# Kernel optimization log

Hardware: AMD Instinct MI355X
Metric: run time of the kernel (lower is better)

Reference implementation:

```python
import jax, jax.numpy as jnp
import numpy as np

OUTCOMES = [8, 8, 8, 8, 8, 8]           # concept outcome counts (concepts_order)
N_TOTAL = int(np.prod(OUTCOMES))        # 262144 joint states
N_VALID = 8192                          # admissible states
B, D = 4096, 1024


def setup_inputs() -> dict:
    key = jax.random.key(0)
    k1, k2 = jax.random.split(key)
    embeddings = jax.random.normal(k1, (B, D), dtype=jnp.float32)
    W = jax.random.normal(k2, (N_VALID, D), dtype=jnp.float32) * 0.02
    b = jnp.zeros((N_VALID,), dtype=jnp.float32)
    # unique sorted admissible-state indices, like torch.argwhere(mask)
    rng = np.random.default_rng(0)
    valid_states = jnp.asarray(
        np.sort(rng.choice(N_TOTAL, size=N_VALID, replace=False)).astype(np.int32))
    return {"embeddings": embeddings, "W": W, "b": b, "valid_states": valid_states}


def reference(embeddings, W, b, valid_states):
    # softmax over valid states: [B, N_VALID]
    probs = jax.nn.softmax(embeddings @ W.T + b, axis=1)
    probs_t = probs.T  # [N_VALID, B] for leading-axis segment reduction
    marginals = []
    stride = N_TOTAL
    for n_i in OUTCOMES:
        stride //= n_i
        # digit of each valid joint-state index along this concept's axis
        digit = (valid_states // stride) % n_i  # [N_VALID]
        # equivalent to scattering probs into the full joint tensor and
        # summing over all other concept axes, without materializing it
        m = jax.ops.segment_sum(probs_t, digit, num_segments=n_i).T  # [B, n_i]
        marginals.append(m)
    return jnp.stack(marginals)  # [n_concepts, B, 8]
```

## Files before the change

### kernel.cpp

```cpp
#include <hip/hip_runtime.h>
#include <hip/hip_bf16.h>
#include <cstdint>
#include <cstddef>

typedef __bf16 bf16_t;
typedef bf16_t bf16x8 __attribute__((ext_vector_type(8)));
typedef bf16_t bf16x4 __attribute__((ext_vector_type(4)));
typedef float  f32x4  __attribute__((ext_vector_type(4)));
typedef unsigned int u32;

#define BROWS 4096
#define NV    8192
#define KD    1024
#define KSPLIT 16
#define NT    16

#define GLL(gsrc, ldst) \
  __builtin_amdgcn_global_load_lds((const __attribute__((address_space(1))) u32*)(gsrc), \
                                   (__attribute__((address_space(3))) u32*)(ldst), 16, 0, 0)
#define FENCE asm volatile("" ::: "memory")

__global__ void cvt_kernel(const float* __restrict__ src, bf16_t* __restrict__ dst, int n4) {
  int idx = blockIdx.x * blockDim.x + threadIdx.x;
  int stride = gridDim.x * blockDim.x;
  for (int i = idx; i < n4; i += stride) {
    float4 v = ((const float4*)src)[i];
    bf16x4 o;
    o[0] = (bf16_t)v.x; o[1] = (bf16_t)v.y; o[2] = (bf16_t)v.z; o[3] = (bf16_t)v.w;
    ((bf16x4*)dst)[i] = o;
  }
}

__global__ void build_st_kernel(const int* __restrict__ vstate, bf16_t* __restrict__ st) {
  int g = blockIdx.x * blockDim.x + threadIdx.x;
  if (g >= 48 * NV) return;
  int bucket = g >> 13;
  int j = g & (NV - 1);
  int c = bucket >> 3;
  int d = bucket & 7;
  int dig = (vstate[j] >> (15 - 3 * c)) & 7;
  st[g] = (bf16_t)(dig == d ? 1.0f : 0.0f);
}

__global__ __launch_bounds__(512, 2)
void gemm_exp_kernel(const bf16_t* __restrict__ A, const bf16_t* __restrict__ B,
                     const float* __restrict__ bias, bf16_t* __restrict__ expout) {
  __shared__ __align__(16) char lds[2][65536];
  #define AKH0 0
  #define AKH1 16384
  #define BKH0 32768
  #define BKH1 49152

  const int t    = threadIdx.x;
  const int lane = t & 63;
  const int wv   = t >> 6;
  const int wm   = wv >> 2;
  const int wn   = wv & 3;
  const int fr   = lane & 15;
  const int fq   = lane >> 4;

  int bid = blockIdx.x;
  int wg  = (bid & 7) * 64 + (bid >> 3);
  const int mt = wg >> 5;
  const int nt = wg & 31;
  const int row0 = mt * 256;
  const int col0 = nt * 256;

  const int srow = lane >> 2;
  const int skel = ((lane & 3) ^ ((lane >> 3) & 3)) * 8;
  const bf16_t* aptr = A + (size_t)(row0 + wv * 32 + srow) * KD + skel;
  const bf16_t* bptr = B + (size_t)(col0 + wv * 32 + srow) * KD + skel;
  const int dchunk = (wv * 2) * 1024;

  const int xsw = (fr & 6) << 3;
  const int base_a = (((wm * 128 + fr) * 64 + fq * 16) ^ xsw);
  const int base_b = 32768 + (((wn * 64 + fr) * 64 + fq * 16) ^ xsw);

  f32x4 acc[8][4] = {};

  GLL(aptr, &lds[0][AKH0 + dchunk]);
  GLL(aptr + 16 * KD, &lds[0][AKH0 + dchunk + 1024]);
  GLL(bptr, &lds[0][BKH0 + dchunk]);
  GLL(bptr + 16 * KD, &lds[0][BKH0 + dchunk + 1024]);
  GLL(aptr + 32, &lds[0][AKH1 + dchunk]);
  GLL(aptr + 32 + 16 * KD, &lds[0][AKH1 + dchunk + 1024]);
  GLL(bptr + 32, &lds[0][BKH1 + dchunk]);
  GLL(bptr + 32 + 16 * KD, &lds[0][BKH1 + dchunk + 1024]);
  asm volatile("s_waitcnt vmcnt(0)" ::: "memory");
  __builtin_amdgcn_s_barrier();
  FENCE;

  int cur = 0;
  for (int kt = 0; kt < NT; ++kt) {
    const char* bufp = lds[cur];
    char* nbuf = lds[cur ^ 1];
    const bool pf = (kt + 1 < NT);

    bf16x8 a0[8], b0[4], a1[8], b1[4];

#pragma unroll
    for (int n = 0; n < 4; ++n)
      b0[n] = *(const bf16x8*)(bufp + base_b + n * 1024);
#pragma unroll
    for (int m = 0; m < 8; ++m)
      a0[m] = *(const bf16x8*)(bufp + base_a + m * 1024);

    if (pf) {
      const bf16_t* an = aptr + (kt + 1) * 64;
      const bf16_t* bn = bptr + (kt + 1) * 64;
      GLL(an, &nbuf[AKH0 + dchunk]);
      GLL(an + 16 * KD, &nbuf[AKH0 + dchunk + 1024]);
      GLL(bn, &nbuf[BKH0 + dchunk]);
      GLL(bn + 16 * KD, &nbuf[BKH0 + dchunk + 1024]);
      GLL(an + 32, &nbuf[AKH1 + dchunk]);
      GLL(an + 32 + 16 * KD, &nbuf[AKH1 + dchunk + 1024]);
      GLL(bn + 32, &nbuf[BKH1 + dchunk]);
      GLL(bn + 32 + 16 * KD, &nbuf[BKH1 + dchunk + 1024]);
    }

#pragma unroll
    for (int n = 0; n < 4; ++n)
      b1[n] = *(const bf16x8*)(bufp + base_b + 16384 + n * 1024);
#pragma unroll
    for (int m = 0; m < 8; ++m)
      a1[m] = *(const bf16x8*)(bufp + base_a + 16384 + m * 1024);

    __builtin_amdgcn_s_setprio(1);
#pragma unroll
    for (int m = 0; m < 8; ++m)
#pragma unroll
      for (int n = 0; n < 4; ++n)
        acc[m][n] = __builtin_amdgcn_mfma_f32_16x16x32_bf16(a0[m], b0[n], acc[m][n], 0, 0, 0);
#pragma unroll
    for (int m = 0; m < 8; ++m)
#pragma unroll
      for (int n = 0; n < 4; ++n)
        acc[m][n] = __builtin_amdgcn_mfma_f32_16x16x32_bf16(a1[m], b1[n], acc[m][n], 0, 0, 0);
    __builtin_amdgcn_s_setprio(0);

    asm volatile("s_waitcnt vmcnt(0)" ::: "memory");
    __builtin_amdgcn_sched_barrier(0);
    __builtin_amdgcn_s_barrier();
    FENCE;
    cur ^= 1;
  }

#pragma unroll
  for (int n = 0; n < 4; ++n) {
    const int col = col0 + wn * 64 + n * 16 + fr;
    const float bb = bias[col];
#pragma unroll
    for (int m = 0; m < 8; ++m) {
      const int rowb = row0 + wm * 128 + m * 16 + fq * 4;
#pragma unroll
      for (int r = 0; r < 4; ++r) {
        float e = exp2f((acc[m][n][r] + bb) * 1.44269504088896340736f);
        expout[(size_t)(rowb + r) * NV + col] = (bf16_t)e;
      }
    }
  }
}

__global__ __launch_bounds__(256)
void marginal_mfma_kernel(const bf16_t* __restrict__ expbuf, const bf16_t* __restrict__ st,
                          float* __restrict__ part) {
  __shared__ bf16_t sE[128][32];
  __shared__ bf16_t sS[48][32];

  const int t    = threadIdx.x;
  const int lane = t & 63;
  const int wv   = t >> 6;

  const int rt = blockIdx.x >> 4;
  const int ks = blockIdx.x & (KSPLIT - 1);
  const int row0 = rt * 128;
  const int kbase = ks * (NV / KSPLIT);

  const int srow = t >> 2;
  const int skel = (t & 3) * 8;
  const bf16_t* ep0 = expbuf + (size_t)(row0 + srow) * NV + kbase + skel;
  const bf16_t* ep1 = ep0 + (size_t)64 * NV;
  const bf16_t* sp0 = st + (size_t)srow * NV + kbase + skel;
  bf16_t* se0 = &sE[0][0] + (wv * 64) * 8;
  bf16_t* se1 = &sE[0][0] + (256 + wv * 64) * 8;
  bf16_t* ss0 = &sS[0][0] + (wv * 64) * 8;

  const int fr = lane & 15;
  const int fq = lane >> 4;

  f32x4 acc[2][3] = {};

  for (int kk = 0; kk < NV / KSPLIT; kk += 32) {
    GLL(ep0 + kk, se0);
    GLL(ep1 + kk, se1);
    if (wv < 3) GLL(sp0 + kk, ss0);
    __syncthreads();

    bf16x8 af[2], bg[3];
#pragma unroll
    for (int m = 0; m < 2; ++m)
      af[m] = *(const bf16x8*)&sE[wv * 32 + m * 16 + fr][fq * 8];
#pragma unroll
    for (int n = 0; n < 3; ++n)
      bg[n] = *(const bf16x8*)&sS[n * 16 + fr][fq * 8];
#pragma unroll
    for (int m = 0; m < 2; ++m)
#pragma unroll
      for (int n = 0; n < 3; ++n)
        acc[m][n] = __builtin_amdgcn_mfma_f32_16x16x32_bf16(af[m], bg[n], acc[m][n], 0, 0, 0);
    __syncthreads();
  }

  float* pbase = part + (size_t)ks * BROWS * 48;
#pragma unroll
  for (int m = 0; m < 2; ++m) {
    const int rowb = row0 + wv * 32 + m * 16 + fq * 4;
#pragma unroll
    for (int n = 0; n < 3; ++n) {
      const int bucket = n * 16 + fr;
#pragma unroll
      for (int r = 0; r < 4; ++r)
        pbase[(size_t)(rowb + r) * 48 + bucket] = acc[m][n][r];
    }
  }
}

__global__ __launch_bounds__(64)
void reduce_kernel(const float* __restrict__ part, float* __restrict__ out) {
  const int b = blockIdx.x;
  const int t = threadIdx.x;
  __shared__ float fin[48];
  if (t < 48) {
    float s = 0.f;
#pragma unroll
    for (int ks = 0; ks < KSPLIT; ++ks)
      s += part[((size_t)ks * BROWS + b) * 48 + t];
    fin[t] = s;
  }
  __syncthreads();
  if (t < 48) {
    float total = fin[0] + fin[1] + fin[2] + fin[3] + fin[4] + fin[5] + fin[6] + fin[7];
    out[(size_t)(t >> 3) * BROWS * 8 + (size_t)b * 8 + (t & 7)] = fin[t] / total;
  }
}

extern "C" void kernel_launch(void* const* d_in, const int* in_sizes, int n_in,
                              void* d_out, int out_size, void* d_ws, size_t ws_size,
                              hipStream_t stream) {
  const float* E    = (const float*)d_in[0];
  const float* W    = (const float*)d_in[1];
  const float* bias = (const float*)d_in[2];
  const int*   vs   = (const int*)d_in[3];
  float* out = (float*)d_out;

  char* ws = (char*)d_ws;
  size_t off = 0;
  bf16_t* Eb     = (bf16_t*)(ws + off); off += (size_t)BROWS * KD * 2;
  bf16_t* Wb     = (bf16_t*)(ws + off); off += (size_t)NV * KD * 2;
  bf16_t* expbuf = (bf16_t*)(ws + off); off += (size_t)BROWS * NV * 2;
  bf16_t* st     = (bf16_t*)(ws + off); off += (size_t)48 * NV * 2;
  float*  part   = (float*)(ws + off);  off += (size_t)KSPLIT * BROWS * 48 * 4;

  build_st_kernel<<<(48 * NV + 255) / 256, 256, 0, stream>>>(vs, st);
  cvt_kernel<<<2048, 256, 0, stream>>>(E, Eb, BROWS * KD / 4);
  cvt_kernel<<<2048, 256, 0, stream>>>(W, Wb, NV * KD / 4);
  gemm_exp_kernel<<<512, 512, 0, stream>>>(Eb, Wb, bias, expbuf);
  marginal_mfma_kernel<<<32 * KSPLIT, 256, 0, stream>>>(expbuf, st, part);
  reduce_kernel<<<BROWS, 64, 0, stream>>>(part, out);
}
```

Before: 119.6 us.

## Fuse exp and marginal MFMA reduction into GEMM epilogue, drop exp buffer

The GEMM is transposed so each block tiles 256 valid states by 256 batch rows. The epilogue writes exp values into LDS in swizzled form and immediately multiplies them against a swizzled one-hot state-to-bucket matrix with MFMA, producing per-state-tile partial marginals. This removes the 64MB bf16 exp buffer round trip and the separate marginal kernel. In exchange the reduce now sums 32 partials per row instead of 16, and the epilogue adds two LDS passes with barriers.

```diff
diff --git a/kernel.cpp b/kernel.cpp
--- a/kernel.cpp
+++ b/kernel.cpp
@@ -12,8 +12,9 @@
 #define BROWS 4096
 #define NV    8192
 #define KD    1024
-#define KSPLIT 16
 #define NT    16
+#define ST    48
+#define LOG2E 1.44269504088896340736f
 
 #define GLL(gsrc, ldst) \
   __builtin_amdgcn_global_load_lds((const __attribute__((address_space(1))) u32*)(gsrc), \
@@ -31,20 +32,22 @@
   }
 }
 
-__global__ void build_st_kernel(const int* __restrict__ vstate, bf16_t* __restrict__ st) {
+__global__ void build_s2t_kernel(const int* __restrict__ vstate, bf16_t* __restrict__ s2t) {
   int g = blockIdx.x * blockDim.x + threadIdx.x;
-  if (g >= 48 * NV) return;
-  int bucket = g >> 13;
-  int j = g & (NV - 1);
-  int c = bucket >> 3;
-  int d = bucket & 7;
-  int dig = (vstate[j] >> (15 - 3 * c)) & 7;
-  st[g] = (bf16_t)(dig == d ? 1.0f : 0.0f);
+  if (g >= ST * NV) return;
+  int b = g >> 13;
+  int ig = g & (NV - 1);
+  int c = b >> 3;
+  int d = b & 7;
+  int src = ig ^ ((b & 7) << 3);
+  int dig = (vstate[src] >> (15 - 3 * c)) & 7;
+  s2t[g] = (bf16_t)(dig == d ? 1.0f : 0.0f);
 }
 
 __global__ __launch_bounds__(512, 2)
-void gemm_exp_kernel(const bf16_t* __restrict__ A, const bf16_t* __restrict__ B,
-                     const float* __restrict__ bias, bf16_t* __restrict__ expout) {
+void gemm_fused_kernel(const bf16_t* __restrict__ W, const bf16_t* __restrict__ E,
+                       const float* __restrict__ bias, const bf16_t* __restrict__ s2t,
+                       float* __restrict__ part) {
   __shared__ __align__(16) char lds[2][65536];
   #define AKH0 0
   #define AKH1 16384
@@ -61,15 +64,15 @@
 
   int bid = blockIdx.x;
   int wg  = (bid & 7) * 64 + (bid >> 3);
-  const int mt = wg >> 5;
-  const int nt = wg & 31;
-  const int row0 = mt * 256;
-  const int col0 = nt * 256;
+  const int stile = wg >> 4;
+  const int btile = wg & 15;
+  const int st0 = stile * 256;
+  const int bt0 = btile * 256;
 
   const int srow = lane >> 2;
   const int skel = ((lane & 3) ^ ((lane >> 3) & 3)) * 8;
-  const bf16_t* aptr = A + (size_t)(row0 + wv * 32 + srow) * KD + skel;
-  const bf16_t* bptr = B + (size_t)(col0 + wv * 32 + srow) * KD + skel;
+  const bf16_t* aptr = W + (size_t)(st0 + wv * 32 + srow) * KD + skel;
+  const bf16_t* bptr = E + (size_t)(bt0 + wv * 32 + srow) * KD + skel;
   const int dchunk = (wv * 2) * 1024;
 
   const int xsw = (fr & 6) << 3;
@@ -145,83 +148,58 @@
     cur ^= 1;
   }
 
-#pragma unroll
-  for (int n = 0; n < 4; ++n) {
-    const int col = col0 + wn * 64 + n * 16 + fr;
-    const float bb = bias[col];
-#pragma unroll
-    for (int m = 0; m < 8; ++m) {
-      const int rowb = row0 + wm * 128 + m * 16 + fq * 4;
-#pragma unroll
-      for (int r = 0; r < 4; ++r) {
-        float e = exp2f((acc[m][n][r] + bb) * 1.44269504088896340736f);
-        expout[(size_t)(rowb + r) * NV + col] = (bf16_t)e;
+  char* const ldsf = &lds[0][0];
+  {
+#pragma unroll
+    for (int q = 0; q < 3; ++q) {
+      const bf16_t* src = s2t + (size_t)(wv * 6 + q * 2 + (lane >> 5)) * NV
+                          + st0 + (lane & 31) * 8;
+      GLL(src, ldsf + 65536 + wv * 3072 + q * 1024);
+    }
+  }
+
+  float* const ppart = part + ((size_t)stile * BROWS + bt0) * ST;
+
+#pragma unroll
+  for (int pass = 0; pass < 2; ++pass) {
+    if ((wn >> 1) == pass) {
+#pragma unroll
+      for (int m = 0; m < 8; ++m) {
+        const float4 bb = *(const float4*)&bias[st0 + wm * 128 + m * 16 + fq * 4];
+#pragma unroll
+        for (int n = 0; n < 4; ++n) {
+          bf16x4 ev;
+          ev[0] = (bf16_t)exp2f((acc[m][n][0] + bb.x) * LOG2E);
+          ev[1] = (bf16_t)exp2f((acc[m][n][1] + bb.y) * LOG2E);
+          ev[2] = (bf16_t)exp2f((acc[m][n][2] + bb.z) * LOG2E);
+          ev[3] = (bf16_t)exp2f((acc[m][n][3] + bb.w) * LOG2E);
+          const int jh = (wn & 1) * 64 + n * 16 + fr;
+          const int ib = (wm * 128 + m * 16 + fq * 4) * 2;
+          *(bf16x4*)(ldsf + jh * 512 + (ib ^ ((fr & 7) << 4))) = ev;
+        }
       }
     }
-  }
-}
-
-__global__ __launch_bounds__(256)
-void marginal_mfma_kernel(const bf16_t* __restrict__ expbuf, const bf16_t* __restrict__ st,
-                          float* __restrict__ part) {
-  __shared__ bf16_t sE[128][32];
-  __shared__ bf16_t sS[48][32];
-
-  const int t    = threadIdx.x;
-  const int lane = t & 63;
-  const int wv   = t >> 6;
-
-  const int rt = blockIdx.x >> 4;
-  const int ks = blockIdx.x & (KSPLIT - 1);
-  const int row0 = rt * 128;
-  const int kbase = ks * (NV / KSPLIT);
-
-  const int srow = t >> 2;
-  const int skel = (t & 3) * 8;
-  const bf16_t* ep0 = expbuf + (size_t)(row0 + srow) * NV + kbase + skel;
-  const bf16_t* ep1 = ep0 + (size_t)64 * NV;
-  const bf16_t* sp0 = st + (size_t)srow * NV + kbase + skel;
-  bf16_t* se0 = &sE[0][0] + (wv * 64) * 8;
-  bf16_t* se1 = &sE[0][0] + (256 + wv * 64) * 8;
-  bf16_t* ss0 = &sS[0][0] + (wv * 64) * 8;
-
-  const int fr = lane & 15;
-  const int fq = lane >> 4;
-
-  f32x4 acc[2][3] = {};
-
-  for (int kk = 0; kk < NV / KSPLIT; kk += 32) {
-    GLL(ep0 + kk, se0);
-    GLL(ep1 + kk, se1);
-    if (wv < 3) GLL(sp0 + kk, ss0);
+    if (pass == 0) asm volatile("s_waitcnt vmcnt(0)" ::: "memory");
     __syncthreads();
 
-    bf16x8 af[2], bg[3];
-#pragma unroll
-    for (int m = 0; m < 2; ++m)
-      af[m] = *(const bf16x8*)&sE[wv * 32 + m * 16 + fr][fq * 8];
-#pragma unroll
-    for (int n = 0; n < 3; ++n)
-      bg[n] = *(const bf16x8*)&sS[n * 16 + fr][fq * 8];
-#pragma unroll
-    for (int m = 0; m < 2; ++m)
-#pragma unroll
-      for (int n = 0; n < 3; ++n)
-        acc[m][n] = __builtin_amdgcn_mfma_f32_16x16x32_bf16(af[m], bg[n], acc[m][n], 0, 0, 0);
+    f32x4 acc2[3] = {{0.f,0.f,0.f,0.f},{0.f,0.f,0.f,0.f},{0.f,0.f,0.f,0.f}};
+#pragma unroll
+    for (int k2 = 0; k2 < 8; ++k2) {
+      const int ko = (k2 * 64 + fq * 16) ^ ((fr & 7) << 4);
+      const bf16x8 ea = *(const bf16x8*)(ldsf + (wv * 16 + fr) * 512 + ko);
+#pragma unroll
+      for (int n2 = 0; n2 < 3; ++n2) {
+        const bf16x8 sb = *(const bf16x8*)(ldsf + 65536 + (n2 * 16 + fr) * 512 + ko);
+        acc2[n2] = __builtin_amdgcn_mfma_f32_16x16x32_bf16(ea, sb, acc2[n2], 0, 0, 0);
+      }
+    }
+    const int jg = pass * 128 + wv * 16 + fq * 4;
+#pragma unroll
+    for (int n2 = 0; n2 < 3; ++n2)
+#pragma unroll
+      for (int r = 0; r < 4; ++r)
+        ppart[(size_t)(jg + r) * ST + n2 * 16 + fr] = acc2[n2][r];
     __syncthreads();
-  }
-
-  float* pbase = part + (size_t)ks * BROWS * 48;
-#pragma unroll
-  for (int m = 0; m < 2; ++m) {
-    const int rowb = row0 + wv * 32 + m * 16 + fq * 4;
-#pragma unroll
-    for (int n = 0; n < 3; ++n) {
-      const int bucket = n * 16 + fr;
-#pragma unroll
-      for (int r = 0; r < 4; ++r)
-        pbase[(size_t)(rowb + r) * 48 + bucket] = acc[m][n][r];
-    }
   }
 }
 
@@ -229,16 +207,16 @@
 void reduce_kernel(const float* __restrict__ part, float* __restrict__ out) {
   const int b = blockIdx.x;
   const int t = threadIdx.x;
-  __shared__ float fin[48];
-  if (t < 48) {
+  __shared__ float fin[ST];
+  if (t < ST) {
     float s = 0.f;
 #pragma unroll
-    for (int ks = 0; ks < KSPLIT; ++ks)
-      s += part[((size_t)ks * BROWS + b) * 48 + t];
+    for (int mt = 0; mt < 32; ++mt)
+      s += part[((size_t)mt * BROWS + b) * ST + t];
     fin[t] = s;
   }
   __syncthreads();
-  if (t < 48) {
+  if (t < ST) {
     float total = fin[0] + fin[1] + fin[2] + fin[3] + fin[4] + fin[5] + fin[6] + fin[7];
     out[(size_t)(t >> 3) * BROWS * 8 + (size_t)b * 8 + (t & 7)] = fin[t] / total;
   }
@@ -255,16 +233,14 @@
 
   char* ws = (char*)d_ws;
   size_t off = 0;
-  bf16_t* Eb     = (bf16_t*)(ws + off); off += (size_t)BROWS * KD * 2;
-  bf16_t* Wb     = (bf16_t*)(ws + off); off += (size_t)NV * KD * 2;
-  bf16_t* expbuf = (bf16_t*)(ws + off); off += (size_t)BROWS * NV * 2;
-  bf16_t* st     = (bf16_t*)(ws + off); off += (size_t)48 * NV * 2;
-  float*  part   = (float*)(ws + off);  off += (size_t)KSPLIT * BROWS * 48 * 4;
-
-  build_st_kernel<<<(48 * NV + 255) / 256, 256, 0, stream>>>(vs, st);
+  bf16_t* Eb   = (bf16_t*)(ws + off); off += (size_t)BROWS * KD * 2;
+  bf16_t* Wb   = (bf16_t*)(ws + off); off += (size_t)NV * KD * 2;
+  bf16_t* s2t  = (bf16_t*)(ws + off); off += (size_t)ST * NV * 2;
+  float*  part = (float*)(ws + off);  off += (size_t)32 * BROWS * ST * 4;
+
+  build_s2t_kernel<<<(ST * NV + 255) / 256, 256, 0, stream>>>(vs, s2t);
   cvt_kernel<<<2048, 256, 0, stream>>>(E, Eb, BROWS * KD / 4);
   cvt_kernel<<<2048, 256, 0, stream>>>(W, Wb, NV * KD / 4);
-  gemm_exp_kernel<<<512, 512, 0, stream>>>(Eb, Wb, bias, expbuf);
-  marginal_mfma_kernel<<<32 * KSPLIT, 256, 0, stream>>>(expbuf, st, part);
+  gemm_fused_kernel<<<512, 512, 0, stream>>>(Wb, Eb, bias, s2t, part);
   reduce_kernel<<<BROWS, 64, 0, stream>>>(part, out);
 }
```

New measurement: 106.2 us. 1.13x faster.
